# Kernel optimization log

Measured on AMD Instinct MI355X. Metric: run time of the kernel, lower is better.

The kernel has to match this reference:

```python
import jax, jax.numpy as jnp
import numpy as np
from jax import lax

N_FREE = 10
DT = 0.1
COMP = 4


def setup_inputs() -> dict:
    key = jax.random.key(0)
    kx, kw = jax.random.split(key)
    B, D = 256, 16384
    nodes = D // COMP  # 4096
    x = jax.random.normal(kx, (B, D), dtype=jnp.float32)
    # Hopfield-style node-coupling matrix (learned parameter), small init for stable relaxation
    W = jax.random.normal(kw, (nodes, nodes), dtype=jnp.float32) * 0.02
    return {"x": x, "W": W}


def reference(x, W):
    B, D = x.shape
    nodes = D // COMP
    # project scalar features to multivectors (B, nodes, comp)
    x_mv = x.reshape(B, nodes, COMP)
    W_sym = 0.5 * (W + W.T)  # symmetric coupling => well-defined energy

    def step(h, _):
        rho = jnp.tanh(h)                                      # (B, nodes, comp)
        drive = jnp.einsum('nm,bmc->bnc', W_sym, rho) + x_mv   # recurrent + input coupling
        grad_E = h - (1.0 - rho * rho) * drive                 # dE/dh
        return h - DT * grad_E, None

    h_free, _ = lax.scan(step, x_mv, None, length=N_FREE)
    return h_free[..., 0]  # scalar (grade-0) component, (B, nodes)
```

## Files before the change

kernel.cpp:

```cpp
#include <hip/hip_runtime.h>
#include <hip/hip_bf16.h>


#define NODES 4096
#define KDIM  4096
#define MDIM  1024
#define DLEN  16384
#define BM 64
#define BN 128
#define BK 32
#define HALF_ELEMS 4194304

typedef __attribute__((ext_vector_type(8))) __bf16 bf16x8;
typedef __attribute__((ext_vector_type(8))) unsigned short u16x8;
typedef __attribute__((ext_vector_type(4))) float  f32x4;

static __device__ __forceinline__ unsigned short f32_to_bf16(float f) {
    unsigned int u = __float_as_uint(f);
    u += 0x7fffu + ((u >> 16) & 1u);
    return (unsigned short)(u >> 16);
}
static __device__ __forceinline__ float bf16_to_f32(unsigned short u) {
    return __uint_as_float(((unsigned int)u) << 16);
}

__global__ __launch_bounds__(256)
void symw_kernel(const float* __restrict__ W, unsigned short* __restrict__ Wbp) {
    __shared__ float Ta[64][64];
    __shared__ float Tb[64][65];
    const int tn = blockIdx.y, tm = blockIdx.x;
    const int c  = threadIdx.x & 63;
    const int r0 = threadIdx.x >> 6;
#pragma unroll
    for (int rr = 0; rr < 16; ++rr) {
        int r = r0 * 16 + rr;
        Ta[r][c] = W[(size_t)(tn * 64 + r) * 4096 + tm * 64 + c];
        Tb[r][c] = W[(size_t)(tm * 64 + r) * 4096 + tn * 64 + c];
    }
    __syncthreads();
#pragma unroll
    for (int rr = 0; rr < 16; ++rr) {
        int r = r0 * 16 + rr;
        float v = 0.5f * (Ta[r][c] + Tb[c][r]);
        int n = tn * 64 + r;
        int k = tm * 64 + c;
        size_t addr = ((size_t)(k >> 5) * 256 + (n >> 4)) * 512
                    + (size_t)((n & 15) | (((k >> 3) & 3) << 4)) * 8 + (k & 7);
        Wbp[addr] = f32_to_bf16(v);
    }
}

__global__ __launch_bounds__(256)
void init_kernel(const float* __restrict__ x, float* __restrict__ h,
                 unsigned short* __restrict__ P0) {
    int idx = blockIdx.x * blockDim.x + threadIdx.x;
    int b = idx >> 12;
    int m = idx & 4095;
    f32x4 xv = *(const f32x4*)(x + (size_t)idx * 4);
    *(f32x4*)(h + (size_t)idx * 4) = xv;
    size_t base = ((size_t)(m >> 5) * 64 + (b >> 2)) * 512
                + (size_t)((m >> 3) & 3) * 128 + (m & 7);
#pragma unroll
    for (int c = 0; c < 4; ++c) {
        P0[base + (size_t)((b & 3) * 4 + c) * 8] = f32_to_bf16(tanhf(xv[c]));
    }
}

__global__ __launch_bounds__(256, 4)
void gemm_kernel(const unsigned short* __restrict__ Pcur,
                 const unsigned short* __restrict__ Wbp,
                 unsigned short* __restrict__ Dp) {
    __shared__ unsigned short Bs[3][BN * BK];

    const int tid  = threadIdx.x;
    const int bx   = blockIdx.x;
    const int by   = blockIdx.y;
    const int ks   = blockIdx.z;
    const int w    = tid >> 6;
    const int lane = tid & 63;
    const int lr   = lane & 15;
    const int lk   = lane >> 4;
    const int m0   = (w >> 1) * 32;
    const int n0   = (w & 1) * 64;
    const int mr0  = by * 4 + (m0 >> 4);
    const int T0   = ks * 64;

    size_t soff[2]; int dsto[2];
#pragma unroll
    for (int j = 0; j < 2; ++j) {
        int c = tid + 256 * j;
        soff[j] = ((size_t)(bx * 8 + (c >> 6))) * 512 + (size_t)(c & 63) * 8;
        dsto[j] = c * 8;
    }
    size_t aoff[2];
#pragma unroll
    for (int mi = 0; mi < 2; ++mi)
        aoff[mi] = (size_t)(mr0 + mi) * 512 + (size_t)lane * 8;
    const int boff = ((w & 1) * 4) * 512 + lane * 8;

    f32x4 acc[2][4];
#pragma unroll
    for (int mi = 0; mi < 2; ++mi)
#pragma unroll
        for (int ni = 0; ni < 4; ++ni)
            acc[mi][ni] = (f32x4){0.f, 0.f, 0.f, 0.f};

    unsigned short* BsF = &Bs[0][0];

#define STAGE(buf, t32)                                                         \
    do {                                                                        \
        _Pragma("unroll")                                                       \
        for (int j = 0; j < 2; ++j) {                                           \
            __builtin_amdgcn_global_load_lds(                                   \
                (const __attribute__((address_space(1))) void*)                \
                    (Wbp + (size_t)(t32) * 131072 + soff[j]),                   \
                (__attribute__((address_space(3))) void*)                      \
                    (BsF + (buf) * 4096 + dsto[j]),                             \
                16, 0, 0);                                                      \
        }                                                                       \
    } while (0)

#define LOADA(s, t32)                                                           \
    do {                                                                        \
        _Pragma("unroll")                                                       \
        for (int mi = 0; mi < 2; ++mi)                                          \
            s[mi] = *(const bf16x8*)(Pcur + (size_t)(t32) * 32768 + aoff[mi]);  \
    } while (0)

#define COMPUTE(buf, s)                                                         \
    do {                                                                        \
        bf16x8 bfr[4];                                                          \
        _Pragma("unroll")                                                       \
        for (int ni = 0; ni < 4; ++ni)                                          \
            bfr[ni] = *(const bf16x8*)(BsF + (buf) * 4096 + boff + ni * 512);   \
        _Pragma("unroll")                                                       \
        for (int mi = 0; mi < 2; ++mi)                                          \
            _Pragma("unroll")                                                   \
            for (int ni = 0; ni < 4; ++ni)                                      \
                acc[mi][ni] = __builtin_amdgcn_mfma_f32_16x16x32_bf16(          \
                    s[mi], bfr[ni], acc[mi][ni], 0, 0, 0);                      \
    } while (0)

    bf16x8 aA[2], aB[2];
    STAGE(0, T0);     LOADA(aA, T0);
    STAGE(1, T0 + 1); LOADA(aB, T0 + 1);

    int c0 = 0, c1 = 1, c2 = 2;
    for (int tp = 0; tp < 31; ++tp) {
        const int t = T0 + 2 * tp;
        asm volatile("s_waitcnt vmcnt(4)" ::: "memory");
        __builtin_amdgcn_s_barrier();
        STAGE(c2, t + 2);
        COMPUTE(c0, aA);
        LOADA(aA, t + 2);
        { int z = c0; c0 = c1; c1 = c2; c2 = z; }
        asm volatile("s_waitcnt vmcnt(4)" ::: "memory");
        __builtin_amdgcn_s_barrier();
        STAGE(c2, t + 3);
        COMPUTE(c0, aB);
        LOADA(aB, t + 3);
        { int z = c0; c0 = c1; c1 = c2; c2 = z; }
    }
    asm volatile("s_waitcnt vmcnt(4)" ::: "memory");
    __builtin_amdgcn_s_barrier();
    COMPUTE(c0, aA);
    { int z = c0; c0 = c1; c1 = c2; c2 = z; }
    asm volatile("s_waitcnt vmcnt(0)" ::: "memory");
    __builtin_amdgcn_s_barrier();
    COMPUTE(c0, aB);
#undef STAGE
#undef LOADA
#undef COMPUTE

    const int rowA0 = by * BM, rowB0 = bx * BN;
    unsigned short* D = Dp + (size_t)ks * HALF_ELEMS;
#pragma unroll
    for (int mi = 0; mi < 2; ++mi) {
        int i0 = rowA0 + m0 + mi * 16 + lk * 4;
#pragma unroll
        for (int ni = 0; ni < 4; ++ni) {
            int n = rowB0 + n0 + ni * 16 + lr;
#pragma unroll
            for (int r = 0; r < 4; ++r)
                D[(size_t)(i0 + r) * NODES + n] = f32_to_bf16(acc[mi][ni][r]);
        }
    }
}

__global__ __launch_bounds__(256)
void combine_kernel(const unsigned short* __restrict__ Dp,
                    const float* __restrict__ x,
                    float* __restrict__ h,
                    unsigned short* __restrict__ Pnxt,
                    float* __restrict__ out) {
    int g  = blockIdx.x * 256 + threadIdx.x;
    int b  = g >> 9;
    int mg = (g & 511) << 3;
    size_t hbase = (size_t)b * DLEN + (size_t)mg * 4;

    f32x4 hv[8], xv[8];
#pragma unroll
    for (int e = 0; e < 8; ++e) {
        hv[e] = *(const f32x4*)(h + hbase + e * 4);
        xv[e] = *(const f32x4*)(x + hbase + e * 4);
    }
    u16x8 d0[4], d1[4];
#pragma unroll
    for (int c = 0; c < 4; ++c) {
        d0[c] = *(const u16x8*)(Dp + (size_t)(b * 4 + c) * NODES + mg);
        d1[c] = *(const u16x8*)(Dp + HALF_ELEMS + (size_t)(b * 4 + c) * NODES + mg);
    }
    u16x8 pn[4];
    float o[8];
#pragma unroll
    for (int e = 0; e < 8; ++e) {
#pragma unroll
        for (int c = 0; c < 4; ++c) {
            float p    = bf16_to_f32(d0[c][e]) + bf16_to_f32(d1[c][e]);
            float hvv  = hv[e][c];
            float rho  = tanhf(hvv);
            float drive = p + xv[e][c];
            float hnew = 0.9f * hvv + 0.1f * (1.0f - rho * rho) * drive;
            hv[e][c] = hnew;
            pn[c][e] = f32_to_bf16(tanhf(hnew));
            if (c == 0) o[e] = hnew;
        }
    }
#pragma unroll
    for (int e = 0; e < 8; ++e)
        *(f32x4*)(h + hbase + e * 4) = hv[e];
#pragma unroll
    for (int c = 0; c < 4; ++c) {
        size_t pa = (size_t)(mg >> 5) * 32768 + (size_t)(b >> 2) * 512
                  + (size_t)(((b & 3) * 4 + c) | (((mg >> 3) & 3) << 4)) * 8;
        *(u16x8*)(Pnxt + pa) = pn[c];
    }
    if (out) {
        *(f32x4*)(out + (size_t)b * NODES + mg)     = (f32x4){o[0], o[1], o[2], o[3]};
        *(f32x4*)(out + (size_t)b * NODES + mg + 4) = (f32x4){o[4], o[5], o[6], o[7]};
    }
}

extern "C" void kernel_launch(void* const* d_in, const int* in_sizes, int n_in,
                              void* d_out, int out_size, void* d_ws, size_t ws_size,
                              hipStream_t stream) {
    const float* x = (const float*)d_in[0];
    const float* W = (const float*)d_in[1];
    float* out = (float*)d_out;

    char* ws = (char*)d_ws;
    unsigned short* Wbp = (unsigned short*)(ws);
    unsigned short* P0  = (unsigned short*)(ws + ((size_t)32 << 20));
    unsigned short* P1  = (unsigned short*)(ws + ((size_t)40 << 20));
    float*          h   = (float*)(ws + ((size_t)48 << 20));
    unsigned short* Dp  = (unsigned short*)(ws + ((size_t)64 << 20));

    symw_kernel<<<dim3(64, 64), 256, 0, stream>>>(W, Wbp);
    init_kernel<<<dim3(4096), 256, 0, stream>>>(x, h, P0);

    unsigned short* pc = P0;
    unsigned short* pn = P1;
    for (int s = 0; s < 10; ++s) {
        gemm_kernel<<<dim3(32, 16, 2), 256, 0, stream>>>(pc, Wbp, Dp);
        combine_kernel<<<dim3(512), 256, 0, stream>>>(
            Dp, x, h, pn, (s == 9) ? out : nullptr);
        unsigned short* t = pc; pc = pn; pn = t;
    }
}
```

Measured before the change: 648.5 us.

## Restructure GEMM into single-wave 64x64 tiles with barrier-free 4-slot LDS pipeline

The GEMM moves from 256-thread blocks with 64x128 tiles to 64-thread single-wavefront blocks computing 64x64 tiles each. Because only one wave uses its private LDS buffers, the s_barrier calls go away. A 4-slot ring with vmcnt waits keeps three B-tile loads in flight. The cost is that W tiles are no longer shared across four waves, so global/L2 traffic for B goes up. The grid also doubles, which changes occupancy, and the clamped tail iterations redo loads that are not needed.

```diff
diff --git a/kernel.cpp b/kernel.cpp
--- a/kernel.cpp
+++ b/kernel.cpp
@@ -6,9 +6,6 @@
 #define KDIM  4096
 #define MDIM  1024
 #define DLEN  16384
-#define BM 64
-#define BN 128
-#define BK 32
 #define HALF_ELEMS 4194304
 
 typedef __attribute__((ext_vector_type(8))) __bf16 bf16x8;
@@ -66,120 +63,112 @@
     }
 }
 
-__global__ __launch_bounds__(256, 4)
+__global__ __launch_bounds__(64, 2)
 void gemm_kernel(const unsigned short* __restrict__ Pcur,
                  const unsigned short* __restrict__ Wbp,
                  unsigned short* __restrict__ Dp) {
-    __shared__ unsigned short Bs[3][BN * BK];
-
-    const int tid  = threadIdx.x;
+    __shared__ unsigned short Bs[4 * 2048];
+
+    const int lane = threadIdx.x;
     const int bx   = blockIdx.x;
     const int by   = blockIdx.y;
     const int ks   = blockIdx.z;
-    const int w    = tid >> 6;
-    const int lane = tid & 63;
-    const int lr   = lane & 15;
-    const int lk   = lane >> 4;
-    const int m0   = (w >> 1) * 32;
-    const int n0   = (w & 1) * 64;
-    const int mr0  = by * 4 + (m0 >> 4);
     const int T0   = ks * 64;
 
-    size_t soff[2]; int dsto[2];
-#pragma unroll
-    for (int j = 0; j < 2; ++j) {
-        int c = tid + 256 * j;
-        soff[j] = ((size_t)(bx * 8 + (c >> 6))) * 512 + (size_t)(c & 63) * 8;
-        dsto[j] = c * 8;
-    }
-    size_t aoff[2];
-#pragma unroll
-    for (int mi = 0; mi < 2; ++mi)
-        aoff[mi] = (size_t)(mr0 + mi) * 512 + (size_t)lane * 8;
-    const int boff = ((w & 1) * 4) * 512 + lane * 8;
-
-    f32x4 acc[2][4];
-#pragma unroll
-    for (int mi = 0; mi < 2; ++mi)
+    size_t soff[4];
+#pragma unroll
+    for (int j = 0; j < 4; ++j)
+        soff[j] = ((size_t)(bx * 4 + j)) * 512 + (size_t)lane * 8;
+    size_t aoff[4];
+#pragma unroll
+    for (int mi = 0; mi < 4; ++mi)
+        aoff[mi] = ((size_t)(by * 4 + mi)) * 512 + (size_t)lane * 8;
+
+    f32x4 acc[4][4];
+#pragma unroll
+    for (int mi = 0; mi < 4; ++mi)
 #pragma unroll
         for (int ni = 0; ni < 4; ++ni)
             acc[mi][ni] = (f32x4){0.f, 0.f, 0.f, 0.f};
 
-    unsigned short* BsF = &Bs[0][0];
-
-#define STAGE(buf, t32)                                                         \
+    bf16x8 aA[4], aB[4];
+
+#define TC(t) ((t) < 63 ? (t) : 63)
+
+#define STAGE(slot, tl)                                                         \
     do {                                                                        \
-        _Pragma("unroll")                                                       \
-        for (int j = 0; j < 2; ++j) {                                           \
+        const unsigned short* src =                                             \
+            Wbp + (size_t)(T0 + (tl)) * 131072;                                 \
+        _Pragma("unroll")                                                       \
+        for (int j = 0; j < 4; ++j) {                                           \
             __builtin_amdgcn_global_load_lds(                                   \
-                (const __attribute__((address_space(1))) void*)                \
-                    (Wbp + (size_t)(t32) * 131072 + soff[j]),                   \
+                (const __attribute__((address_space(1))) void*)(src + soff[j]), \
                 (__attribute__((address_space(3))) void*)                      \
-                    (BsF + (buf) * 4096 + dsto[j]),                             \
+                    (Bs + (slot) * 2048 + j * 512 + lane * 8),                  \
                 16, 0, 0);                                                      \
         }                                                                       \
     } while (0)
 
-#define LOADA(s, t32)                                                           \
+#define LOADA(s, tl)                                                            \
     do {                                                                        \
-        _Pragma("unroll")                                                       \
-        for (int mi = 0; mi < 2; ++mi)                                          \
-            s[mi] = *(const bf16x8*)(Pcur + (size_t)(t32) * 32768 + aoff[mi]);  \
+        const unsigned short* Pt = Pcur + (size_t)(T0 + (tl)) * 32768;          \
+        _Pragma("unroll")                                                       \
+        for (int mi = 0; mi < 4; ++mi)                                          \
+            s[mi] = *(const bf16x8*)(Pt + aoff[mi]);                            \
     } while (0)
 
-#define COMPUTE(buf, s)                                                         \
+#define COMPUTE(slot, s)                                                        \
     do {                                                                        \
+        const unsigned short* Bb = Bs + (slot) * 2048;                          \
         bf16x8 bfr[4];                                                          \
         _Pragma("unroll")                                                       \
         for (int ni = 0; ni < 4; ++ni)                                          \
-            bfr[ni] = *(const bf16x8*)(BsF + (buf) * 4096 + boff + ni * 512);   \
-        _Pragma("unroll")                                                       \
-        for (int mi = 0; mi < 2; ++mi)                                          \
+            bfr[ni] = *(const bf16x8*)(Bb + ni * 512 + lane * 8);               \
+        _Pragma("unroll")                                                       \
+        for (int mi = 0; mi < 4; ++mi)                                          \
             _Pragma("unroll")                                                   \
             for (int ni = 0; ni < 4; ++ni)                                      \
                 acc[mi][ni] = __builtin_amdgcn_mfma_f32_16x16x32_bf16(          \
                     s[mi], bfr[ni], acc[mi][ni], 0, 0, 0);                      \
     } while (0)
 
-    bf16x8 aA[2], aB[2];
-    STAGE(0, T0);     LOADA(aA, T0);
-    STAGE(1, T0 + 1); LOADA(aB, T0 + 1);
-
-    int c0 = 0, c1 = 1, c2 = 2;
+    STAGE(0, 0);
+    LOADA(aA, 0);
+    STAGE(1, 1);
+    STAGE(2, 2);
+    LOADA(aB, 1);
+    STAGE(3, 3);
+    asm volatile("s_waitcnt vmcnt(16)" ::: "memory");
+    COMPUTE(0, aA);
+
     for (int tp = 0; tp < 31; ++tp) {
-        const int t = T0 + 2 * tp;
-        asm volatile("s_waitcnt vmcnt(4)" ::: "memory");
-        __builtin_amdgcn_s_barrier();
-        STAGE(c2, t + 2);
-        COMPUTE(c0, aA);
-        LOADA(aA, t + 2);
-        { int z = c0; c0 = c1; c1 = c2; c2 = z; }
-        asm volatile("s_waitcnt vmcnt(4)" ::: "memory");
-        __builtin_amdgcn_s_barrier();
-        STAGE(c2, t + 3);
-        COMPUTE(c0, aB);
-        LOADA(aB, t + 3);
-        { int z = c0; c0 = c1; c1 = c2; c2 = z; }
-    }
-    asm volatile("s_waitcnt vmcnt(4)" ::: "memory");
-    __builtin_amdgcn_s_barrier();
-    COMPUTE(c0, aA);
-    { int z = c0; c0 = c1; c1 = c2; c2 = z; }
+        const int t = 1 + 2 * tp;
+        LOADA(aA, TC(t + 1));
+        STAGE((t + 3) & 3, TC(t + 3));
+        asm volatile("s_waitcnt vmcnt(12)" ::: "memory");
+        COMPUTE(t & 3, aB);
+
+        const int u = t + 1;
+        LOADA(aB, TC(u + 1));
+        STAGE((u + 3) & 3, TC(u + 3));
+        asm volatile("s_waitcnt vmcnt(12)" ::: "memory");
+        COMPUTE(u & 3, aA);
+    }
     asm volatile("s_waitcnt vmcnt(0)" ::: "memory");
-    __builtin_amdgcn_s_barrier();
-    COMPUTE(c0, aB);
+    COMPUTE(3, aB);
 #undef STAGE
 #undef LOADA
 #undef COMPUTE
-
-    const int rowA0 = by * BM, rowB0 = bx * BN;
+#undef TC
+
+    const int lr = lane & 15, lk = lane >> 4;
     unsigned short* D = Dp + (size_t)ks * HALF_ELEMS;
 #pragma unroll
-    for (int mi = 0; mi < 2; ++mi) {
-        int i0 = rowA0 + m0 + mi * 16 + lk * 4;
+    for (int mi = 0; mi < 4; ++mi) {
+        int i0 = by * 64 + mi * 16 + lk * 4;
 #pragma unroll
         for (int ni = 0; ni < 4; ++ni) {
-            int n = rowB0 + n0 + ni * 16 + lr;
+            int n = bx * 64 + ni * 16 + lr;
 #pragma unroll
             for (int r = 0; r < 4; ++r)
                 D[(size_t)(i0 + r) * NODES + n] = f32_to_bf16(acc[mi][ni][r]);
@@ -261,7 +250,7 @@
     unsigned short* pc = P0;
     unsigned short* pn = P1;
     for (int s = 0; s < 10; ++s) {
-        gemm_kernel<<<dim3(32, 16, 2), 256, 0, stream>>>(pc, Wbp, Dp);
+        gemm_kernel<<<dim3(64, 16, 2), 64, 0, stream>>>(pc, Wbp, Dp);
         combine_kernel<<<dim3(512), 256, 0, stream>>>(
             Dp, x, h, pn, (s == 9) ? out : nullptr);
         unsigned short* t = pc; pc = pn; pn = t;
```

Measured after the change: 653.9 us. Within noise of the previous version (+0.8%).
